# Kernel optimization log

Hardware: AMD Instinct MI355X
Metric: run time of the kernel (lower is better)

Reference implementation:

```python
import jax, jax.numpy as jnp
import numpy as np

LAYERS, HIDDEN, FFN, HEADS = 2, 128, 256, 4
IMG_H, IMG_W = 32, 64
SEQ = IMG_H * IMG_W
HEAD = HIDDEN // HEADS          # 32, per-head qk dim
HEAD_V = 2 * HEAD               # double_v_dim=True
VDIM = HEADS * HEAD_V           # 256
B = 2
SCALE_BASE = 512.0
EPS = 1e-5


def _xpos_tables(seq, d):
    # XPOS: rotary angles + per-position exponential scale
    half = d // 2
    scale_vec = (jnp.arange(0, d, 2, dtype=jnp.float32) + 0.4 * d) / (1.4 * d)  # (d/2,)
    power = jnp.arange(seq, dtype=jnp.float32) / SCALE_BASE
    scale = scale_vec[None, :] ** power[:, None]                                 # (S, d/2)
    inv_freq = 1.0 / (10000.0 ** (jnp.arange(half, dtype=jnp.float32) / half))
    ang = jnp.arange(seq, dtype=jnp.float32)[:, None] * inv_freq[None, :]        # (S, d/2)
    return jnp.sin(ang), jnp.cos(ang), scale


def _apply_xpos(x, sin, cos, scale):
    # duplicate-interleave sin/cos*scale to width d, rotate-every-two
    s = jnp.repeat(sin * scale, 2, axis=-1)   # (S, d)
    c = jnp.repeat(cos * scale, 2, axis=-1)
    x1, x2 = x[..., ::2], x[..., 1::2]
    rot = jnp.stack([-x2, x1], axis=-1).reshape(x.shape)
    return x * c + rot * s


def _ln(x, g, b):
    mu = x.mean(-1, keepdims=True)
    var = ((x - mu) ** 2).mean(-1, keepdims=True)
    return (x - mu) * jax.lax.rsqrt(var + EPS) * g + b


def _gn(y, g, b):
    # GroupNorm(HEADS groups) over VDIM channels, applied per token
    bsz, s, v = y.shape
    yg = y.reshape(bsz, s, HEADS, HEAD_V)
    mu = yg.mean(-1, keepdims=True)
    var = ((yg - mu) ** 2).mean(-1, keepdims=True)
    yn = ((yg - mu) * jax.lax.rsqrt(var + EPS)).reshape(bsz, s, v)
    return yn * g + b


def _decay(seq):
    # D[h, n, m] = gamma_h^(n-m) for n >= m else 0
    gammas = 1.0 - jnp.exp(jnp.linspace(jnp.log(1.0 / 32.0), jnp.log(1.0 / 512.0), HEADS))
    n = jnp.arange(seq, dtype=jnp.float32)
    diff = n[:, None] - n[None, :]
    return (gammas[:, None, None] ** jnp.maximum(diff, 0.0)) * (diff >= 0.0)


def _forward(x, ln1_g, ln1_b, ln2_g, ln2_b, WQ, WK, WV, WG, WO, gn_g, gn_b, w1, b1, w2, b2):
    sin, cos, scale = _xpos_tables(SEQ, HEAD)
    D = _decay(SEQ)  # (H, S, S)
    for i in range(LAYERS):
        h = _ln(x, ln1_g[i], ln1_b[i])
        Q = _apply_xpos(jnp.einsum('bsd,hde->bhse', h, WQ[i]), sin, cos, scale)
        K = _apply_xpos(jnp.einsum('bsd,hde->bhse', h, WK[i]), sin, cos, 1.0 / scale)
        V = jnp.einsum('bsd,hdv->bhsv', h, WV[i])
        att = jnp.einsum('bhse,bhte->bhst', Q, K) * D[None]      # decay retention
        Y = jnp.einsum('bhst,bhtv->bhsv', att, V)
        Y = jnp.moveaxis(Y, 1, 2).reshape(x.shape[0], SEQ, VDIM)  # concat heads
        Y = _gn(Y, gn_g[i], gn_b[i])
        G = h @ WG[i]
        ret = (G * jax.nn.sigmoid(G) * Y) @ WO[i]                 # swish gate + out proj
        y = ret + x
        h2 = _ln(y, ln2_g[i], ln2_b[i])
        x = jax.nn.gelu(h2 @ w1[i] + b1[i], approximate=False) @ w2[i] + b2[i] + y
    return x.reshape(x.shape[0], IMG_H, IMG_W, x.shape[-1])


def setup_inputs() -> dict:
    key = jax.random.key(0)
    ks = jax.random.split(key, 8)
    def rn(k, shape, sc):
        return jax.random.normal(k, shape, dtype=jnp.float32) * sc
    s = 1.0 / np.sqrt(HIDDEN)
    return {
        'x': rn(ks[0], (B, SEQ, HIDDEN), 1.0),
        'ln1_g': jnp.ones((LAYERS, HIDDEN), jnp.float32),
        'ln1_b': jnp.zeros((LAYERS, HIDDEN), jnp.float32),
        'ln2_g': jnp.ones((LAYERS, HIDDEN), jnp.float32),
        'ln2_b': jnp.zeros((LAYERS, HIDDEN), jnp.float32),
        'WQ': rn(ks[1], (LAYERS, HEADS, HIDDEN, HEAD), s),
        'WK': rn(ks[2], (LAYERS, HEADS, HIDDEN, HEAD), s),
        'WV': rn(ks[3], (LAYERS, HEADS, HIDDEN, HEAD_V), s),
        'WG': rn(ks[4], (LAYERS, HIDDEN, VDIM), s),
        'WO': rn(ks[5], (LAYERS, VDIM, HIDDEN), 1.0 / np.sqrt(VDIM)),
        'gn_g': jnp.ones((LAYERS, VDIM), jnp.float32),
        'gn_b': jnp.zeros((LAYERS, VDIM), jnp.float32),
        'w1': rn(ks[6], (LAYERS, HIDDEN, FFN), s),
        'b1': jnp.zeros((LAYERS, FFN), jnp.float32),
        'w2': rn(ks[7], (LAYERS, FFN, HIDDEN), 1.0 / np.sqrt(FFN)),
        'b2': jnp.zeros((LAYERS, HIDDEN), jnp.float32),
    }


def reference(x, ln1_g, ln1_b, ln2_g, ln2_b, WQ, WK, WV, WG, WO, gn_g, gn_b, w1, b1, w2, b2):
    return _forward(x, ln1_g, ln1_b, ln2_g, ln2_b, WQ, WK, WV, WG, WO, gn_g, gn_b, w1, b1, w2, b2)
```

## Files before the change

kernel.cpp:

```cpp
#include <hip/hip_runtime.h>
#include <math.h>

#define NLAYERS 2
#define HID 128
#define FFND 256
#define NH 4
#define SEQL 2048
#define HD 32
#define HDV 64
#define VD 256
#define NBATCH 2
#define MROWS (NBATCH*SEQL)
#define NCAT 768
#define NCHUNK 32

__global__ __launch_bounds__(256) void pack_w_kernel(
    const float* __restrict__ WQ, const float* __restrict__ WK,
    const float* __restrict__ WV, const float* __restrict__ WG,
    float* __restrict__ Wcat)
{
  int idx = blockIdx.x * 256 + threadIdx.x;
  if (idx >= NLAYERS * HID * NCAT) return;
  int l = idx / (HID * NCAT);
  int r = idx - l * (HID * NCAT);
  int k = r / NCAT;
  int n = r - k * NCAT;
  float v;
  if (n < 128)      { int h = n >> 5, e = n & 31;          v = WQ[(((l*NH+h)*HID)+k)*HD  + e]; }
  else if (n < 256) { int m = n-128; int h = m>>5, e = m&31; v = WK[(((l*NH+h)*HID)+k)*HD  + e]; }
  else if (n < 512) { int m = n-256; int h = m>>6, e = m&63; v = WV[(((l*NH+h)*HID)+k)*HDV + e]; }
  else              { v = WG[(l*HID + k)*VD + (n-512)]; }
  Wcat[idx] = v;
}

__global__ __launch_bounds__(256) void xpos_tables_kernel(float* __restrict__ tabs)
{
  int idx = blockIdx.x * 256 + threadIdx.x;
  if (idx >= SEQL * 16) return;
  int s = idx >> 4, i = idx & 15;
  float inv_freq = powf(10000.f, -(float)i * (1.f/16.f));
  float ang = (float)s * inv_freq;
  float sv  = ((float)(2*i) + 0.4f*32.f) / (1.4f*32.f);
  float sc  = powf(sv, (float)s * (1.f/512.f));
  float sn = sinf(ang), cs = cosf(ang);
  tabs[idx]          = sn * sc;
  tabs[32768 + idx]  = cs * sc;
  tabs[65536 + idx]  = sn / sc;
  tabs[98304 + idx]  = cs / sc;
}

__global__ __launch_bounds__(256) void ln_rows_kernel(
    const float* __restrict__ X, const float* __restrict__ g,
    const float* __restrict__ b, float* __restrict__ O)
{
  int wid = threadIdx.x >> 6, lane = threadIdx.x & 63;
  int row = blockIdx.x * 4 + wid;
  const float* x = X + (size_t)row * HID;
  float v0 = x[lane], v1 = x[lane + 64];
  float s = v0 + v1;
  #pragma unroll
  for (int o = 32; o; o >>= 1) s += __shfl_xor(s, o);
  float mu = s * (1.f/128.f);
  float d0 = v0 - mu, d1 = v1 - mu;
  float q = d0*d0 + d1*d1;
  #pragma unroll
  for (int o = 32; o; o >>= 1) q += __shfl_xor(q, o);
  float rs = rsqrtf(q * (1.f/128.f) + 1e-5f);
  O[(size_t)row*HID + lane]      = d0 * rs * g[lane]      + b[lane];
  O[(size_t)row*HID + lane + 64] = d1 * rs * g[lane + 64] + b[lane + 64];
}

template<int KTOT, bool BIAS, bool RESID, bool GELU, bool XPOS>
__global__ __launch_bounds__(256) void gemm64(
    const float* __restrict__ A, const float* __restrict__ Bw,
    const float* __restrict__ bias, const float* __restrict__ Rsd,
    const float* __restrict__ tabs, float* __restrict__ C, int N)
{
  __shared__ float As[64][68];
  __shared__ float Bs[64][68];
  int tid = threadIdx.x;
  int tx = tid & 15, ty = tid >> 4;
  int rb = blockIdx.x * 64, nb = blockIdx.y * 64;

  float acc[4][4];
  #pragma unroll
  for (int i=0;i<4;i++)
    #pragma unroll
    for (int j=0;j<4;j++) acc[i][j] = 0.f;

  for (int ks = 0; ks < KTOT; ks += 64) {
    #pragma unroll
    for (int it = 0; it < 4; it++) {
      int idx = it*256 + tid;
      int row = idx >> 4, kq = idx & 15;
      float4 a4 = *(const float4*)(A + (size_t)(rb+row)*KTOT + ks + 4*kq);
      int rsw = row ^ (4*(kq & 7));
      As[4*kq+0][rsw] = a4.x; As[4*kq+1][rsw] = a4.y;
      As[4*kq+2][rsw] = a4.z; As[4*kq+3][rsw] = a4.w;
    }
    #pragma unroll
    for (int it = 0; it < 4; it++) {
      int idx = it*256 + tid;
      int kk = idx >> 4, nq = idx & 15;
      *(float4*)(&Bs[kk][4*nq]) = *(const float4*)(Bw + (size_t)(ks+kk)*N + nb + 4*nq);
    }
    __syncthreads();
    #pragma unroll
    for (int k = 0; k < 64; k++) {
      float a[4], bv[4];
      *(float4*)a  = *(const float4*)&As[k][(4*ty) ^ (4*((k>>2)&7))];
      *(float4*)bv = *(const float4*)&Bs[k][4*tx];
      #pragma unroll
      for (int i=0;i<4;i++)
        #pragma unroll
        for (int j=0;j<4;j++)
          acc[i][j] = fmaf(a[i], bv[j], acc[i][j]);
    }
    __syncthreads();
  }

  #pragma unroll
  for (int i=0;i<4;i++) {
    int row = rb + 4*ty + i;
    float o[4];
    #pragma unroll
    for (int j=0;j<4;j++) {
      int col = nb + 4*tx + j;
      float v = acc[i][j];
      if (BIAS)  v += bias[col];
      if (GELU)  v = 0.5f * v * (1.f + erff(v * 0.70710678118f));
      if (RESID) v += Rsd[(size_t)row*N + col];
      o[j] = v;
    }
    if (XPOS) {
      if (nb < 256) {
        bool isK = (nb >= 128);
        const float* sn_t = tabs + (isK ? 65536 : 0);
        const float* cs_t = tabs + (isK ? 98304 : 32768);
        int s = row & (SEQL - 1);
        int cb = nb + 4*tx;
        int i0 = (cb & 31) >> 1;
        float sn0 = sn_t[s*16 + i0],     cs0 = cs_t[s*16 + i0];
        float sn1 = sn_t[s*16 + i0 + 1], cs1 = cs_t[s*16 + i0 + 1];
        float x1 = o[0], x2 = o[1];
        o[0] = x1*cs0 - x2*sn0;  o[1] = x2*cs0 + x1*sn0;
        x1 = o[2]; x2 = o[3];
        o[2] = x1*cs1 - x2*sn1;  o[3] = x2*cs1 + x1*sn1;
      }
    }
    *(float4*)(C + (size_t)row*N + nb + 4*tx) = *(float4*)o;
  }
}

__global__ __launch_bounds__(256) void ret_kv_kernel(
    const float* __restrict__ QKVG, float* __restrict__ Asum)
{
  int bh = blockIdx.x >> 5;
  int c  = blockIdx.x & 31;
  int b = bh >> 2, h = bh & 3;
  float t0 = logf(1.f/32.f) + (float)h * (logf(1.f/512.f) - logf(1.f/32.f)) * (1.f/3.f);
  float gamma = 1.f - expf(t0);
  float lg = logf(gamma);

  __shared__ float Ks[64][36];
  __shared__ float Vs[64][68];
  __shared__ float wt[64];

  int tid = threadIdx.x;
  int c0 = c * 64;
  const float* base = QKVG + (size_t)(b * SEQL) * NCAT;

  #pragma unroll
  for (int it = 0; it < 2; it++) {
    int idx = it*256 + tid;
    int row = idx >> 3, eq = idx & 7;
    *(float4*)&Ks[row][4*eq] =
        *(const float4*)(base + (size_t)(c0+row)*NCAT + 128 + h*32 + 4*eq);
  }
  #pragma unroll
  for (int it = 0; it < 4; it++) {
    int idx = it*256 + tid;
    int row = idx >> 4, vq = idx & 15;
    *(float4*)&Vs[row][4*vq] =
        *(const float4*)(base + (size_t)(c0+row)*NCAT + 256 + h*64 + 4*vq);
  }
  if (tid < 64) wt[tid] = __expf(lg * (float)(64 - tid));
  __syncthreads();

  int e = tid >> 3, v8 = (tid & 7) * 8;
  float a0[4] = {0,0,0,0}, a1[4] = {0,0,0,0};
  #pragma unroll 4
  for (int t = 0; t < 64; t++) {
    float kw = Ks[t][e] * wt[t];
    float4 v0 = *(const float4*)&Vs[t][v8];
    float4 v1 = *(const float4*)&Vs[t][v8+4];
    a0[0] = fmaf(kw, v0.x, a0[0]); a0[1] = fmaf(kw, v0.y, a0[1]);
    a0[2] = fmaf(kw, v0.z, a0[2]); a0[3] = fmaf(kw, v0.w, a0[3]);
    a1[0] = fmaf(kw, v1.x, a1[0]); a1[1] = fmaf(kw, v1.y, a1[1]);
    a1[2] = fmaf(kw, v1.z, a1[2]); a1[3] = fmaf(kw, v1.w, a1[3]);
  }
  float* ob = Asum + ((size_t)(bh*NCHUNK + c))*2048 + e*64 + v8;
  *(float4*)ob     = *(float4*)a0;
  *(float4*)(ob+4) = *(float4*)a1;
}

__global__ __launch_bounds__(256) void ret_out_kernel(
    const float* __restrict__ QKVG, const float* __restrict__ Asum,
    const float* __restrict__ gn_g, const float* __restrict__ gn_b,
    float* __restrict__ Gated)
{
  int bh = blockIdx.x >> 5;
  int c  = blockIdx.x & 31;
  int b = bh >> 2, h = bh & 3;
  float t0 = logf(1.f/32.f) + (float)h * (logf(1.f/512.f) - logf(1.f/32.f)) * (1.f/3.f);
  float gamma = 1.f - expf(t0);
  float lg = logf(gamma);
  float g64 = __expf(lg * 64.f);

  __shared__ float Qs[64][36];
  __shared__ float Ks[64][36];
  __shared__ float Vs[64][68];
  __shared__ float Ss[64][68];
  __shared__ float Sc[32][68];

  int tid = threadIdx.x, tx = tid & 15, ty = tid >> 4;
  int c0 = c * 64;
  const float* base = QKVG + (size_t)(b * SEQL) * NCAT;

  #pragma unroll
  for (int it = 0; it < 2; it++) {
    int idx = it*256 + tid;
    int row = idx >> 3, eq = idx & 7;
    *(float4*)&Qs[row][4*eq] =
        *(const float4*)(base + (size_t)(c0+row)*NCAT + h*32 + 4*eq);
    int esw = (4*eq) ^ (4*((row >> 2) & 7));
    *(float4*)&Ks[row][esw] =
        *(const float4*)(base + (size_t)(c0+row)*NCAT + 128 + h*32 + 4*eq);
  }
  #pragma unroll
  for (int it = 0; it < 4; it++) {
    int idx = it*256 + tid;
    int row = idx >> 4, vq = idx & 15;
    *(float4*)&Vs[row][4*vq] =
        *(const float4*)(base + (size_t)(c0+row)*NCAT + 256 + h*64 + 4*vq);
  }

  {
    int e = tid >> 3, v8 = (tid & 7) * 8;
    float s0[4] = {0,0,0,0}, s1[4] = {0,0,0,0};
    float w = 1.f;
    const float* ab = Asum + ((size_t)bh*NCHUNK)*2048 + e*64 + v8;
    for (int cp = c-1; cp >= 0; --cp) {
      const float* ap = ab + (size_t)cp*2048;
      float4 x0 = *(const float4*)ap;
      float4 x1 = *(const float4*)(ap+4);
      s0[0] = fmaf(w, x0.x, s0[0]); s0[1] = fmaf(w, x0.y, s0[1]);
      s0[2] = fmaf(w, x0.z, s0[2]); s0[3] = fmaf(w, x0.w, s0[3]);
      s1[0] = fmaf(w, x1.x, s1[0]); s1[1] = fmaf(w, x1.y, s1[1]);
      s1[2] = fmaf(w, x1.z, s1[2]); s1[3] = fmaf(w, x1.w, s1[3]);
      w *= g64;
    }
    *(float4*)&Sc[e][v8]   = *(float4*)s0;
    *(float4*)&Sc[e][v8+4] = *(float4*)s1;
  }
  __syncthreads();

  float sacc[4][4];
  #pragma unroll
  for (int i=0;i<4;i++)
    #pragma unroll
    for (int j=0;j<4;j++) sacc[i][j] = 0.f;
  #pragma unroll
  for (int e = 0; e < 32; e += 4) {
    float qv[4][4], kv[4][4];
    #pragma unroll
    for (int i=0;i<4;i++)
      *(float4*)qv[i] = *(const float4*)&Qs[4*ty+i][e];
    int esw = e ^ (4*(tx & 7));
    #pragma unroll
    for (int j=0;j<4;j++)
      *(float4*)kv[j] = *(const float4*)&Ks[4*tx+j][esw];
    #pragma unroll
    for (int i=0;i<4;i++)
      #pragma unroll
      for (int j=0;j<4;j++)
        sacc[i][j] = fmaf(qv[i][0], kv[j][0],
                     fmaf(qv[i][1], kv[j][1],
                     fmaf(qv[i][2], kv[j][2],
                     fmaf(qv[i][3], kv[j][3], sacc[i][j]))));
  }
  #pragma unroll
  for (int i=0;i<4;i++) {
    int sl = 4*ty + i;
    float o4[4];
    #pragma unroll
    for (int j=0;j<4;j++) {
      int dr = sl - (4*tx + j);
      float w = (dr >= 0) ? __expf(lg * (float)dr) : 0.f;
      o4[j] = sacc[i][j] * w;
    }
    *(float4*)&Ss[sl][4*tx] = *(float4*)o4;
  }

  float acc[4][4];
  #pragma unroll
  for (int i=0;i<4;i++)
    #pragma unroll
    for (int j=0;j<4;j++) acc[i][j] = 0.f;
  #pragma unroll
  for (int e = 0; e < 32; e += 4) {
    float qv[4][4], sv[4][4];
    #pragma unroll
    for (int i=0;i<4;i++)
      *(float4*)qv[i] = *(const float4*)&Qs[4*ty+i][e];
    #pragma unroll
    for (int m=0;m<4;m++)
      *(float4*)sv[m] = *(const float4*)&Sc[e+m][4*tx];
    #pragma unroll
    for (int i=0;i<4;i++)
      #pragma unroll
      for (int j=0;j<4;j++)
        acc[i][j] = fmaf(qv[i][0], sv[0][j],
                    fmaf(qv[i][1], sv[1][j],
                    fmaf(qv[i][2], sv[2][j],
                    fmaf(qv[i][3], sv[3][j], acc[i][j]))));
  }
  #pragma unroll
  for (int i=0;i<4;i++) {
    float gr = __expf(lg * (float)(4*ty + i));
    #pragma unroll
    for (int j=0;j<4;j++) acc[i][j] *= gr;
  }
  __syncthreads();

  #pragma unroll
  for (int t = 0; t < 64; t += 4) {
    float sv[4][4], vv[4][4];
    #pragma unroll
    for (int i=0;i<4;i++)
      *(float4*)sv[i] = *(const float4*)&Ss[4*ty+i][t];
    #pragma unroll
    for (int m=0;m<4;m++)
      *(float4*)vv[m] = *(const float4*)&Vs[t+m][4*tx];
    #pragma unroll
    for (int i=0;i<4;i++)
      #pragma unroll
      for (int j=0;j<4;j++)
        acc[i][j] = fmaf(sv[i][0], vv[0][j],
                    fmaf(sv[i][1], vv[1][j],
                    fmaf(sv[i][2], vv[2][j],
                    fmaf(sv[i][3], vv[3][j], acc[i][j]))));
  }

  #pragma unroll
  for (int i=0;i<4;i++) {
    float s1 = acc[i][0] + acc[i][1] + acc[i][2] + acc[i][3];
    #pragma unroll
    for (int o = 8; o; o >>= 1) s1 += __shfl_xor(s1, o);
    float mu = s1 * (1.f/64.f);
    float q = 0.f;
    #pragma unroll
    for (int j=0;j<4;j++) { float d = acc[i][j] - mu; q += d*d; }
    #pragma unroll
    for (int o = 8; o; o >>= 1) q += __shfl_xor(q, o);
    float rs = rsqrtf(q * (1.f/64.f) + 1e-5f);
    int row = b*SEQL + c0 + 4*ty + i;
    float4 g4 = *(const float4*)(QKVG + (size_t)row*NCAT + 512 + h*64 + 4*tx);
    float gv[4] = {g4.x, g4.y, g4.z, g4.w};
    float o4[4];
    #pragma unroll
    for (int j=0;j<4;j++) {
      int col = h*64 + 4*tx + j;
      float yn = (acc[i][j] - mu) * rs * gn_g[col] + gn_b[col];
      float g = gv[j];
      float sig = 1.f / (1.f + __expf(-g));
      o4[j] = g * sig * yn;
    }
    *(float4*)(Gated + (size_t)row*VD + h*64 + 4*tx) = *(float4*)o4;
  }
}

extern "C" void kernel_launch(void* const* d_in, const int* in_sizes, int n_in,
                              void* d_out, int out_size, void* d_ws, size_t ws_size,
                              hipStream_t stream)
{
  (void)in_sizes; (void)n_in; (void)out_size; (void)ws_size;
  const float* x_in  = (const float*)d_in[0];
  const float* ln1_g = (const float*)d_in[1];
  const float* ln1_b = (const float*)d_in[2];
  const float* ln2_g = (const float*)d_in[3];
  const float* ln2_b = (const float*)d_in[4];
  const float* WQ    = (const float*)d_in[5];
  const float* WK    = (const float*)d_in[6];
  const float* WV    = (const float*)d_in[7];
  const float* WG    = (const float*)d_in[8];
  const float* WO    = (const float*)d_in[9];
  const float* gn_g  = (const float*)d_in[10];
  const float* gn_b  = (const float*)d_in[11];
  const float* w1    = (const float*)d_in[12];
  const float* b1    = (const float*)d_in[13];
  const float* w2    = (const float*)d_in[14];
  const float* b2    = (const float*)d_in[15];
  float* out = (float*)d_out;
  float* ws  = (float*)d_ws;

  float* Wcat = ws;
  float* tabs = Wcat + 196608;
  float* Hbuf = tabs + 131072;
  float* QKVG = Hbuf + 524288;
  float* Asum = QKVG + 3145728;
  float* Gt   = Asum + 524288;
  float* Yres = Gt   + 1048576;
  float* Mid  = Yres + 524288;

  pack_w_kernel<<<768, 256, 0, stream>>>(WQ, WK, WV, WG, Wcat);
  xpos_tables_kernel<<<128, 256, 0, stream>>>(tabs);

  for (int l = 0; l < NLAYERS; l++) {
    const float* xl = (l == 0) ? x_in : out;
    ln_rows_kernel<<<MROWS/4, 256, 0, stream>>>(xl, ln1_g + l*HID, ln1_b + l*HID, Hbuf);
    gemm64<128,false,false,false,true><<<dim3(MROWS/64, NCAT/64), 256, 0, stream>>>(
        Hbuf, Wcat + l*HID*NCAT, nullptr, nullptr, tabs, QKVG, NCAT);
    ret_kv_kernel<<<256, 256, 0, stream>>>(QKVG, Asum);
    ret_out_kernel<<<256, 256, 0, stream>>>(QKVG, Asum, gn_g + l*VD, gn_b + l*VD, Gt);
    gemm64<256,false,true,false,false><<<dim3(MROWS/64, HID/64), 256, 0, stream>>>(
        Gt, WO + l*VD*HID, nullptr, xl, nullptr, Yres, HID);
    ln_rows_kernel<<<MROWS/4, 256, 0, stream>>>(Yres, ln2_g + l*HID, ln2_b + l*HID, Hbuf);
    gemm64<128,true,false,true,false><<<dim3(MROWS/64, FFND/64), 256, 0, stream>>>(
        Hbuf, w1 + l*HID*FFND, b1 + l*FFND, nullptr, nullptr, Mid, FFND);
    gemm64<256,true,true,false,false><<<dim3(MROWS/64, HID/64), 256, 0, stream>>>(
        Mid, w2 + l*FFND*HID, b2 + l*HID, Yres, nullptr, out, HID);
  }
}
```

Before: 235.5 us.

## Fuse LayerNorm into GEMM prologue, merge setup kernels, narrow N tiles for K=256 GEMMs

LayerNorm is now computed inside the GEMM prologue, with the full 64x128 normalized A tile held in shared memory. This removes the separate ln_rows kernels and the round trip through the Hbuf intermediate. Weight packing and XPOS table generation are merged into one setup launch. The N=128 output GEMMs switch to 32-wide N tiles so they launch twice as many blocks, at the cost of recomputing LayerNorm once per N-tile block and less register reuse per thread.

```diff
diff --git a/kernel.cpp b/kernel.cpp
--- a/kernel.cpp
+++ b/kernel.cpp
@@ -14,90 +14,94 @@
 #define NCAT 768
 #define NCHUNK 32
 
-__global__ __launch_bounds__(256) void pack_w_kernel(
+__global__ __launch_bounds__(256) void setup_kernel(
     const float* __restrict__ WQ, const float* __restrict__ WK,
     const float* __restrict__ WV, const float* __restrict__ WG,
-    float* __restrict__ Wcat)
+    float* __restrict__ Wcat, float* __restrict__ tabs)
 {
-  int idx = blockIdx.x * 256 + threadIdx.x;
-  if (idx >= NLAYERS * HID * NCAT) return;
-  int l = idx / (HID * NCAT);
-  int r = idx - l * (HID * NCAT);
-  int k = r / NCAT;
-  int n = r - k * NCAT;
-  float v;
-  if (n < 128)      { int h = n >> 5, e = n & 31;          v = WQ[(((l*NH+h)*HID)+k)*HD  + e]; }
-  else if (n < 256) { int m = n-128; int h = m>>5, e = m&31; v = WK[(((l*NH+h)*HID)+k)*HD  + e]; }
-  else if (n < 512) { int m = n-256; int h = m>>6, e = m&63; v = WV[(((l*NH+h)*HID)+k)*HDV + e]; }
-  else              { v = WG[(l*HID + k)*VD + (n-512)]; }
-  Wcat[idx] = v;
+  int bid = blockIdx.x;
+  if (bid < 768) {
+    int idx = bid * 256 + threadIdx.x;
+    int l = idx / (HID * NCAT);
+    int r = idx - l * (HID * NCAT);
+    int k = r / NCAT;
+    int n = r - k * NCAT;
+    float v;
+    if (n < 128)      { int h = n >> 5, e = n & 31;            v = WQ[(((l*NH+h)*HID)+k)*HD  + e]; }
+    else if (n < 256) { int m = n-128; int h = m>>5, e = m&31; v = WK[(((l*NH+h)*HID)+k)*HD  + e]; }
+    else if (n < 512) { int m = n-256; int h = m>>6, e = m&63; v = WV[(((l*NH+h)*HID)+k)*HDV + e]; }
+    else              { v = WG[(l*HID + k)*VD + (n-512)]; }
+    Wcat[idx] = v;
+  } else {
+    int idx = (bid - 768) * 256 + threadIdx.x;
+    int s = idx >> 4, i = idx & 15;
+    float inv_freq = powf(10000.f, -(float)i * (1.f/16.f));
+    float ang = (float)s * inv_freq;
+    float sv  = ((float)(2*i) + 0.4f*32.f) / (1.4f*32.f);
+    float sc  = powf(sv, (float)s * (1.f/512.f));
+    float sn = sinf(ang), cs = cosf(ang);
+    tabs[idx]          = sn * sc;
+    tabs[32768 + idx]  = cs * sc;
+    tabs[65536 + idx]  = sn / sc;
+    tabs[98304 + idx]  = cs / sc;
+  }
 }
 
-__global__ __launch_bounds__(256) void xpos_tables_kernel(float* __restrict__ tabs)
+template<bool XPOS, bool BIAS, bool GELU>
+__global__ __launch_bounds__(256) void gemm_ln(
+    const float* __restrict__ A, const float* __restrict__ Bw,
+    const float* __restrict__ lng, const float* __restrict__ lnb,
+    const float* __restrict__ bias, const float* __restrict__ tabs,
+    float* __restrict__ C, int N)
 {
-  int idx = blockIdx.x * 256 + threadIdx.x;
-  if (idx >= SEQL * 16) return;
-  int s = idx >> 4, i = idx & 15;
-  float inv_freq = powf(10000.f, -(float)i * (1.f/16.f));
-  float ang = (float)s * inv_freq;
-  float sv  = ((float)(2*i) + 0.4f*32.f) / (1.4f*32.f);
-  float sc  = powf(sv, (float)s * (1.f/512.f));
-  float sn = sinf(ang), cs = cosf(ang);
-  tabs[idx]          = sn * sc;
-  tabs[32768 + idx]  = cs * sc;
-  tabs[65536 + idx]  = sn / sc;
-  tabs[98304 + idx]  = cs / sc;
-}
-
-__global__ __launch_bounds__(256) void ln_rows_kernel(
-    const float* __restrict__ X, const float* __restrict__ g,
-    const float* __restrict__ b, float* __restrict__ O)
-{
-  int wid = threadIdx.x >> 6, lane = threadIdx.x & 63;
-  int row = blockIdx.x * 4 + wid;
-  const float* x = X + (size_t)row * HID;
-  float v0 = x[lane], v1 = x[lane + 64];
-  float s = v0 + v1;
-  #pragma unroll
-  for (int o = 32; o; o >>= 1) s += __shfl_xor(s, o);
-  float mu = s * (1.f/128.f);
-  float d0 = v0 - mu, d1 = v1 - mu;
-  float q = d0*d0 + d1*d1;
-  #pragma unroll
-  for (int o = 32; o; o >>= 1) q += __shfl_xor(q, o);
-  float rs = rsqrtf(q * (1.f/128.f) + 1e-5f);
-  O[(size_t)row*HID + lane]      = d0 * rs * g[lane]      + b[lane];
-  O[(size_t)row*HID + lane + 64] = d1 * rs * g[lane + 64] + b[lane + 64];
-}
-
-template<int KTOT, bool BIAS, bool RESID, bool GELU, bool XPOS>
-__global__ __launch_bounds__(256) void gemm64(
-    const float* __restrict__ A, const float* __restrict__ Bw,
-    const float* __restrict__ bias, const float* __restrict__ Rsd,
-    const float* __restrict__ tabs, float* __restrict__ C, int N)
-{
-  __shared__ float As[64][68];
+  __shared__ float As[128][68];
   __shared__ float Bs[64][68];
   int tid = threadIdx.x;
   int tx = tid & 15, ty = tid >> 4;
   int rb = blockIdx.x * 64, nb = blockIdx.y * 64;
 
+  {
+    int row = tid >> 2, q = tid & 3;
+    const float* ar = A + (size_t)(rb + row) * HID + 32 * q;
+    float4 av[8];
+    #pragma unroll
+    for (int it = 0; it < 8; it++) av[it] = *(const float4*)(ar + 4*it);
+    float s = 0.f;
+    #pragma unroll
+    for (int it = 0; it < 8; it++) s += av[it].x + av[it].y + av[it].z + av[it].w;
+    s += __shfl_xor(s, 1); s += __shfl_xor(s, 2);
+    float mu = s * (1.f/128.f);
+    float qs = 0.f;
+    #pragma unroll
+    for (int it = 0; it < 8; it++) {
+      float d;
+      d = av[it].x - mu; qs += d*d;  d = av[it].y - mu; qs += d*d;
+      d = av[it].z - mu; qs += d*d;  d = av[it].w - mu; qs += d*d;
+    }
+    qs += __shfl_xor(qs, 1); qs += __shfl_xor(qs, 2);
+    float rs = rsqrtf(qs * (1.f/128.f) + 1e-5f);
+    #pragma unroll
+    for (int it = 0; it < 8; it++) {
+      int k0 = 32*q + 4*it;
+      float4 g4 = *(const float4*)(lng + k0);
+      float4 b4 = *(const float4*)(lnb + k0);
+      float vv[4] = { (av[it].x-mu)*rs*g4.x + b4.x, (av[it].y-mu)*rs*g4.y + b4.y,
+                      (av[it].z-mu)*rs*g4.z + b4.z, (av[it].w-mu)*rs*g4.w + b4.w };
+      #pragma unroll
+      for (int d = 0; d < 4; d++) {
+        int k = k0 + d;
+        As[k][row ^ (4*((k>>2)&7)) ^ (16*((k>>5)&1))] = vv[d];
+      }
+    }
+  }
+
   float acc[4][4];
   #pragma unroll
   for (int i=0;i<4;i++)
     #pragma unroll
     for (int j=0;j<4;j++) acc[i][j] = 0.f;
 
-  for (int ks = 0; ks < KTOT; ks += 64) {
-    #pragma unroll
-    for (int it = 0; it < 4; it++) {
-      int idx = it*256 + tid;
-      int row = idx >> 4, kq = idx & 15;
-      float4 a4 = *(const float4*)(A + (size_t)(rb+row)*KTOT + ks + 4*kq);
-      int rsw = row ^ (4*(kq & 7));
-      As[4*kq+0][rsw] = a4.x; As[4*kq+1][rsw] = a4.y;
-      As[4*kq+2][rsw] = a4.z; As[4*kq+3][rsw] = a4.w;
-    }
+  for (int ks = 0; ks < 128; ks += 64) {
     #pragma unroll
     for (int it = 0; it < 4; it++) {
       int idx = it*256 + tid;
@@ -106,10 +110,11 @@
     }
     __syncthreads();
     #pragma unroll
-    for (int k = 0; k < 64; k++) {
+    for (int kk = 0; kk < 64; kk++) {
+      int k = ks + kk;
       float a[4], bv[4];
-      *(float4*)a  = *(const float4*)&As[k][(4*ty) ^ (4*((k>>2)&7))];
-      *(float4*)bv = *(const float4*)&Bs[k][4*tx];
+      *(float4*)a  = *(const float4*)&As[k][(4*ty) ^ (4*((k>>2)&7)) ^ (16*((k>>5)&1))];
+      *(float4*)bv = *(const float4*)&Bs[kk][4*tx];
       #pragma unroll
       for (int i=0;i<4;i++)
         #pragma unroll
@@ -129,7 +134,6 @@
       float v = acc[i][j];
       if (BIAS)  v += bias[col];
       if (GELU)  v = 0.5f * v * (1.f + erff(v * 0.70710678118f));
-      if (RESID) v += Rsd[(size_t)row*N + col];
       o[j] = v;
     }
     if (XPOS) {
@@ -147,6 +151,71 @@
         x1 = o[2]; x2 = o[3];
         o[2] = x1*cs1 - x2*sn1;  o[3] = x2*cs1 + x1*sn1;
       }
+    }
+    *(float4*)(C + (size_t)row*N + nb + 4*tx) = *(float4*)o;
+  }
+}
+
+template<bool BIAS>
+__global__ __launch_bounds__(256) void gemm_n32(
+    const float* __restrict__ A, const float* __restrict__ Bw,
+    const float* __restrict__ bias, const float* __restrict__ Rsd,
+    float* __restrict__ C, int N)
+{
+  __shared__ float As[64][68];
+  __shared__ float Bs[64][36];
+  int tid = threadIdx.x;
+  int tx = tid & 7, ty = tid >> 3;
+  int rb = blockIdx.x * 64, nb = blockIdx.y * 32;
+
+  float acc[2][4];
+  #pragma unroll
+  for (int i=0;i<2;i++)
+    #pragma unroll
+    for (int j=0;j<4;j++) acc[i][j] = 0.f;
+
+  for (int ks = 0; ks < 256; ks += 64) {
+    #pragma unroll
+    for (int it = 0; it < 4; it++) {
+      int idx = it*256 + tid;
+      int row = idx >> 4, kq = idx & 15;
+      float4 a4 = *(const float4*)(A + (size_t)(rb+row)*256 + ks + 4*kq);
+      int rsw = row ^ (4*(kq & 7));
+      As[4*kq+0][rsw] = a4.x; As[4*kq+1][rsw] = a4.y;
+      As[4*kq+2][rsw] = a4.z; As[4*kq+3][rsw] = a4.w;
+    }
+    #pragma unroll
+    for (int it = 0; it < 2; it++) {
+      int idx = it*256 + tid;
+      int kk = idx >> 3, nq = idx & 7;
+      *(float4*)(&Bs[kk][4*nq]) = *(const float4*)(Bw + (size_t)(ks+kk)*N + nb + 4*nq);
+    }
+    __syncthreads();
+    #pragma unroll
+    for (int k = 0; k < 64; k++) {
+      float2 a2 = *(const float2*)&As[k][(2*ty) ^ (4*((k>>2)&7))];
+      float bv[4];
+      *(float4*)bv = *(const float4*)&Bs[k][4*tx];
+      #pragma unroll
+      for (int j=0;j<4;j++) {
+        acc[0][j] = fmaf(a2.x, bv[j], acc[0][j]);
+        acc[1][j] = fmaf(a2.y, bv[j], acc[1][j]);
+      }
+    }
+    __syncthreads();
+  }
+
+  #pragma unroll
+  for (int i=0;i<2;i++) {
+    int row = rb + 2*ty + i;
+    float o[4];
+    #pragma unroll
+    for (int j=0;j<4;j++) {
+      int col = nb + 4*tx + j;
+      float v = acc[i][j];
+      if (BIAS) v += bias[col];
+      v += Rsd[(size_t)row*N + col];
+      o[j] = v;
     }
     *(float4*)(C + (size_t)row*N + nb + 4*tx) = *(float4*)o;
   }
@@ -406,29 +475,27 @@
 
   float* Wcat = ws;
   float* tabs = Wcat + 196608;
-  float* Hbuf = tabs + 131072;
-  float* QKVG = Hbuf + 524288;
+  float* QKVG = tabs + 131072;
   float* Asum = QKVG + 3145728;
   float* Gt   = Asum + 524288;
   float* Yres = Gt   + 1048576;
   float* Mid  = Yres + 524288;
 
-  pack_w_kernel<<<768, 256, 0, stream>>>(WQ, WK, WV, WG, Wcat);
-  xpos_tables_kernel<<<128, 256, 0, stream>>>(tabs);
+  setup_kernel<<<896, 256, 0, stream>>>(WQ, WK, WV, WG, Wcat, tabs);
 
   for (int l = 0; l < NLAYERS; l++) {
     const float* xl = (l == 0) ? x_in : out;
-    ln_rows_kernel<<<MROWS/4, 256, 0, stream>>>(xl, ln1_g + l*HID, ln1_b + l*HID, Hbuf);
-    gemm64<128,false,false,false,true><<<dim3(MROWS/64, NCAT/64), 256, 0, stream>>>(
-        Hbuf, Wcat + l*HID*NCAT, nullptr, nullptr, tabs, QKVG, NCAT);
+    gemm_ln<true,false,false><<<dim3(MROWS/64, NCAT/64), 256, 0, stream>>>(
+        xl, Wcat + l*HID*NCAT, ln1_g + l*HID, ln1_b + l*HID,
+        nullptr, tabs, QKVG, NCAT);
     ret_kv_kernel<<<256, 256, 0, stream>>>(QKVG, Asum);
     ret_out_kernel<<<256, 256, 0, stream>>>(QKVG, Asum, gn_g + l*VD, gn_b + l*VD, Gt);
-    gemm64<256,false,true,false,false><<<dim3(MROWS/64, HID/64), 256, 0, stream>>>(
-        Gt, WO + l*VD*HID, nullptr, xl, nullptr, Yres, HID);
-    ln_rows_kernel<<<MROWS/4, 256, 0, stream>>>(Yres, ln2_g + l*HID, ln2_b + l*HID, Hbuf);
-    gemm64<128,true,false,true,false><<<dim3(MROWS/64, FFND/64), 256, 0, stream>>>(
-        Hbuf, w1 + l*HID*FFND, b1 + l*FFND, nullptr, nullptr, Mid, FFND);
-    gemm64<256,true,true,false,false><<<dim3(MROWS/64, HID/64), 256, 0, stream>>>(
-        Mid, w2 + l*FFND*HID, b2 + l*HID, Yres, nullptr, out, HID);
+    gemm_n32<false><<<dim3(MROWS/64, HID/32), 256, 0, stream>>>(
+        Gt, WO + l*VD*HID, nullptr, xl, Yres, HID);
+    gemm_ln<false,true,true><<<dim3(MROWS/64, FFND/64), 256, 0, stream>>>(
+        Yres, w1 + l*HID*FFND, ln2_g + l*HID, ln2_b + l*HID,
+        b1 + l*FFND, nullptr, Mid, FFND);
+    gemm_n32<true><<<dim3(MROWS/64, HID/32), 256, 0, stream>>>(
+        Mid, w2 + l*FFND*HID, b2 + l*HID, Yres, out, HID);
   }
 }
```

New measurement: 236.8 us. About the same (+0.6%).
